# Performance work log

Hardware: AMD Instinct MI355X
Metric: run time of the kernel (lower is better)

Reference implementation:

```python
import math
import jax, jax.numpy as jnp
import numpy as np

B, T, C = 2, 2048, 1024
H = 16
HD = C // H
WIN = 33
HALF = WIN // 2
CAUSAL = True
RADIUS, OMEGA, KSPR, STEP = 6.0, 1.0, 1.0, 0.1
EPS = 1e-8


def _spiral_step(x):
    # x: (..., 3) — the stacked (q, k, v) axis; D=3 -> rotate (x0, x1) pair.
    r = jnp.maximum(jnp.linalg.norm(x, axis=-1, keepdims=True), EPS)
    radial = (RADIUS - r) * (x / r)
    c = jnp.float32(math.cos(OMEGA * STEP))
    s = jnp.float32(math.sin(OMEGA * STEP))
    xi, xj, xl = x[..., 0], x[..., 1], x[..., 2]
    y = jnp.stack([c * xi - s * xj, s * xi + c * xj, xl], axis=-1)
    return x + STEP * (y - x + KSPR * radial)


def setup_inputs() -> dict:
    key = jax.random.key(0)
    ks = jax.random.split(key, 3)
    x = jax.random.normal(ks[0], (B, T, C), dtype=jnp.float32)
    W_attn = jax.random.normal(ks[1], (C, 3 * C), dtype=jnp.float32) * (1.0 / math.sqrt(C))
    W_proj = jax.random.normal(ks[2], (C, C), dtype=jnp.float32) * (1.0 / math.sqrt(C))
    sinks = jnp.zeros((H,), dtype=jnp.float32)
    ln_scale = jnp.ones((1,), dtype=jnp.float32) * 0.9
    ln_delta = jnp.ones((C,), dtype=jnp.float32)
    ln_bias = jnp.zeros((C,), dtype=jnp.float32)
    return {"x": x, "W_attn": W_attn, "W_proj": W_proj, "sinks": sinks,
            "ln_scale": ln_scale, "ln_delta": ln_delta, "ln_bias": ln_bias}


def reference(x, W_attn, W_proj, sinks, ln_scale, ln_delta, ln_bias):
    qkv = x @ W_attn                              # (B,T,3C)
    q, k, v = jnp.split(qkv, 3, axis=-1)          # each (B,T,C)

    # SpiralMix over the stacked (q,k,v) axis, loop_iters=2. Only q,k are
    # taken from the mixed output (v stays the pre-spiral value), matching src.
    s = jnp.stack([q, k, v], axis=-1)             # (B,T,C,3)
    s = _spiral_step(_spiral_step(s))
    q, k = s[..., 0], s[..., 1]

    def to_heads(t):
        return t.reshape(B, T, H, HD).transpose(0, 2, 1, 3)  # (B,H,T,hd)
    q, k, v = to_heads(q), to_heads(k), to_heads(v)

    # local window index
    t_idx = jnp.arange(T)
    offs = jnp.arange(-HALF, HALF + 1)
    neigh = t_idx[:, None] + offs[None, :]                    # (T,W)
    valid = (neigh >= 0) & (neigh < T)
    if CAUSAL:
        valid &= neigh <= t_idx[:, None]
    neigh_c = jnp.clip(neigh, 0, T - 1)

    k_n = k[:, :, neigh_c, :]                                 # (B,H,T,W,hd)
    v_n = v[:, :, neigh_c, :]

    inv_sqrt_d = 1.0 / math.sqrt(HD)
    scores = jnp.einsum('bhtd,bhtwd->bhtw',
                        q.astype(jnp.float32), k_n.astype(jnp.float32)) * inv_sqrt_d
    scores = jnp.where(valid[None, None], scores, -jnp.inf)

    # softmax with learned sink logits per head
    sinks_b = sinks.reshape(1, H, 1, 1).astype(scores.dtype)
    m = jnp.max(scores, axis=-1, keepdims=True)
    mj = jnp.maximum(m, sinks_b)
    exp_s = jnp.exp(scores - mj)
    denom = jnp.sum(exp_s, axis=-1, keepdims=True) + jnp.exp(sinks_b - mj)
    att = exp_s / denom                                       # (B,H,T,W)

    y = jnp.einsum('bhtw,bhtwd->bhtd', att, v_n.astype(att.dtype))
    y = y.transpose(0, 2, 1, 3).reshape(B, T, C).astype(x.dtype)
    y = y @ W_proj
    y = jnp.tanh(ln_scale * y)
    return ln_delta * y + ln_bias
```

## Files before the change

kernel.cpp:

```cpp
#include <hip/hip_runtime.h>
#include <hip/hip_fp16.h>
#include <math.h>

#define T_DIM 2048
#define B_DIM 2
#define C_DIM 1024
#define H_DIM 16
#define M_DIM 4096

typedef _Float16 f16x8 __attribute__((ext_vector_type(8)));
typedef _Float16 f16x4 __attribute__((ext_vector_type(4)));
typedef _Float16 f16x2 __attribute__((ext_vector_type(2)));
typedef float    f32x4 __attribute__((ext_vector_type(4)));

#if defined(__has_builtin)
#  if __has_builtin(__builtin_amdgcn_fdot2)
#    define HAVE_FDOT2 1
#  endif
#endif

static __device__ __forceinline__ float FDOT2(f16x2 a, f16x2 b, float c)
{
#ifdef HAVE_FDOT2
    return __builtin_amdgcn_fdot2(a, b, c, false);
#else
    return c + (float)a[0] * (float)b[0] + (float)a[1] * (float)b[1];
#endif
}

#define ASYNC_COPY16(gsrc, ldst) \
  __builtin_amdgcn_global_load_lds( \
    (__attribute__((address_space(1))) unsigned int*)(gsrc), \
    (__attribute__((address_space(3))) unsigned int*)(ldst), 16, 0, 0)

__global__ __launch_bounds__(256) void conv_x_kernel(const float* __restrict__ x,
                                                     _Float16* __restrict__ xh, int n4)
{
    int i = blockIdx.x * 256 + threadIdx.x;
    if (i >= n4) return;
    float4 v = ((const float4*)x)[i];
    f16x4 o;
    o[0] = (_Float16)v.x; o[1] = (_Float16)v.y;
    o[2] = (_Float16)v.z; o[3] = (_Float16)v.w;
    ((f16x4*)xh)[i] = o;
}

__global__ __launch_bounds__(256) void transpose_f16_kernel(const float* __restrict__ W,
                                                            _Float16* __restrict__ WT,
                                                            int K, int N)
{
    __shared__ float tile[32][33];
    const int nbk = K >> 5;
    const int bk = blockIdx.x % nbk;
    const int bn = blockIdx.x / nbk;
    const int tx = threadIdx.x & 31, ty = threadIdx.x >> 5;
#pragma unroll
    for (int r = ty; r < 32; r += 8)
        tile[r][tx] = W[(long)(bk * 32 + r) * N + bn * 32 + tx];
    __syncthreads();
#pragma unroll
    for (int r = ty; r < 32; r += 8)
        WT[(long)(bn * 32 + r) * K + bk * 32 + tx] = (_Float16)tile[tx][r];
}

template<int EPI>
__global__ __launch_bounds__(256) void gemm_f16_kernel(
    const _Float16* __restrict__ A, const _Float16* __restrict__ Bt,
    float* __restrict__ C, int M, int N, int K,
    const float* __restrict__ ln_scale, const float* __restrict__ ln_delta,
    const float* __restrict__ ln_bias)
{
    __shared__ __attribute__((aligned(16))) _Float16 As[128 * 32];
    __shared__ __attribute__((aligned(16))) _Float16 Bs[128 * 32];

    const int tid  = threadIdx.x;
    const int lane = tid & 63;
    const int wave = tid >> 6;
    const int wr = wave >> 1, wc = wave & 1;
    const int ntn = N >> 7;
    const int m0 = (blockIdx.x / ntn) << 7;
    const int n0 = (blockIdx.x % ntn) << 7;

    f32x4 acc[4][4] = {};

    const int off0 = (wave << 10) + (lane << 4);
    const int e0 = off0 >> 1;
    const int e1 = e0 + 2048;
    const int r0 = e0 >> 5, c0 = e0 & 31;
    const int r1 = r0 + 64, c1 = c0;

    const _Float16* a0 = A  + (long)(m0 + r0) * K + c0;
    const _Float16* a1 = A  + (long)(m0 + r1) * K + c1;
    const _Float16* b0 = Bt + (long)(n0 + r0) * K + c0;
    const _Float16* b1 = Bt + (long)(n0 + r1) * K + c1;

    const int fr = lane & 15;
    const int kb = (lane >> 4) << 3;

    for (int k0 = 0; k0 < K; k0 += 32) {
        __syncthreads();
        ASYNC_COPY16(a0 + k0, As + e0);
        ASYNC_COPY16(a1 + k0, As + e1);
        ASYNC_COPY16(b0 + k0, Bs + e0);
        ASYNC_COPY16(b1 + k0, Bs + e1);
        __syncthreads();

        f16x8 af[4], bf[4];
#pragma unroll
        for (int i = 0; i < 4; i++)
            af[i] = *(const f16x8*)&As[(((wr << 6) + (i << 4) + fr) << 5) + kb];
#pragma unroll
        for (int j = 0; j < 4; j++)
            bf[j] = *(const f16x8*)&Bs[(((wc << 6) + (j << 4) + fr) << 5) + kb];
#pragma unroll
        for (int i = 0; i < 4; i++)
#pragma unroll
            for (int j = 0; j < 4; j++)
                acc[i][j] = __builtin_amdgcn_mfma_f32_16x16x32_f16(af[i], bf[j], acc[i][j], 0, 0, 0);
    }

    const int rsub = (lane >> 4) << 2;
    const float lsc = EPI ? ln_scale[0] : 0.f;
#pragma unroll
    for (int j = 0; j < 4; j++) {
        const int col = n0 + (wc << 6) + (j << 4) + fr;
        float ld = 0.f, lb = 0.f;
        if (EPI) { ld = ln_delta[col]; lb = ln_bias[col]; }
#pragma unroll
        for (int i = 0; i < 4; i++) {
            const int rbase = m0 + (wr << 6) + (i << 4) + rsub;
#pragma unroll
            for (int r = 0; r < 4; r++) {
                float v = acc[i][j][r];
                if (EPI) v = ld * tanhf(lsc * v) + lb;
                C[(long)(rbase + r) * N + col] = v;
            }
        }
    }
}

__device__ __forceinline__ void spiral2(float& xi, float& xj, float xl)
{
    const float CS = 0.9950041652780258f;
    const float SN = 0.09983341664682815f;
#pragma unroll
    for (int s = 0; s < 2; s++) {
        float r = sqrtf(xi * xi + xj * xj + xl * xl);
        r = fmaxf(r, 1e-8f);
        const float coef = (6.0f - r) / r;
        const float yi = CS * xi - SN * xj;
        const float yj = SN * xi + CS * xj;
        const float nxi = xi + 0.1f * (yi - xi + coef * xi);
        const float nxj = xj + 0.1f * (yj - xj + coef * xj);
        const float nxl = xl + 0.1f * (coef * xl);
        xi = nxi; xj = nxj; xl = nxl;
    }
}

#define TB   128
#define ROWS 144
#define LDR  68

__global__ __launch_bounds__(128) void attn_kernel(const float* __restrict__ qkv,
                                                   const float* __restrict__ sinks,
                                                   _Float16* __restrict__ yh)
{
    __shared__ __attribute__((aligned(16))) _Float16 k_lds[ROWS * LDR];
    __shared__ __attribute__((aligned(16))) _Float16 v_lds[ROWS * LDR];
    __shared__ __attribute__((aligned(16))) _Float16 q_lds[TB * LDR];

    const int tid = threadIdx.x;
    const int chunk = blockIdx.x & 15;
    const int h = (blockIdx.x >> 4) & 15;
    const int b = blockIdx.x >> 8;
    const int t0 = chunk * TB;
    const long bT = (long)b * T_DIM;

    for (int s = tid; s < ROWS * 4; s += 128) {
        const int ri = s >> 2, q4 = s & 3;
        const int gr = min(max(t0 - 16 + ri, 0), T_DIM - 1);
        const float* base = qkv + (bT + gr) * 3072 + (h << 6) + (q4 << 4);
        float qq[16], kk[16], vv[16];
#pragma unroll
        for (int u = 0; u < 4; u++) {
            *(float4*)&qq[u * 4] = *(const float4*)(base + u * 4);
            *(float4*)&kk[u * 4] = *(const float4*)(base + 1024 + u * 4);
            *(float4*)&vv[u * 4] = *(const float4*)(base + 2048 + u * 4);
        }
#pragma unroll
        for (int u = 0; u < 16; u++) spiral2(qq[u], kk[u], vv[u]);
        const int lbase = ri * LDR + (q4 << 4);
#pragma unroll
        for (int u = 0; u < 8; u++) {
            f16x2 kp; kp[0] = (_Float16)kk[2 * u]; kp[1] = (_Float16)kk[2 * u + 1];
            *(f16x2*)&k_lds[lbase + 2 * u] = kp;
            f16x2 vp; vp[0] = (_Float16)vv[2 * u]; vp[1] = (_Float16)vv[2 * u + 1];
            *(f16x2*)&v_lds[lbase + 2 * u] = vp;
        }
        if (ri >= 16) {
            const int qbase = (ri - 16) * LDR + (q4 << 4);
#pragma unroll
            for (int u = 0; u < 8; u++) {
                f16x2 qp;
                qp[0] = (_Float16)(qq[2 * u] * 0.125f);
                qp[1] = (_Float16)(qq[2 * u + 1] * 0.125f);
                *(f16x2*)&q_lds[qbase + 2 * u] = qp;
            }
        }
    }
    __syncthreads();

    float sc[17];
#pragma unroll
    for (int j = 0; j < 17; j++) sc[j] = 0.f;
    {
        const _Float16* qrow = &q_lds[tid * LDR];
        const _Float16* krow = &k_lds[tid * LDR];
        for (int dd = 0; dd < 32; ++dd) {
            f16x2 q2 = *(const f16x2*)(qrow + 2 * dd);
#pragma unroll
            for (int j = 0; j < 17; j++) {
                f16x2 k2 = *(const f16x2*)(krow + j * LDR + 2 * dd);
                sc[j] = FDOT2(q2, k2, sc[j]);
            }
        }
    }
    __syncthreads();

    const int t = t0 + tid;
#pragma unroll
    for (int j = 0; j < 17; j++)
        if (j + t < 16) sc[j] = -INFINITY;
    const float sink = sinks[h];
    float m = sink;
#pragma unroll
    for (int j = 0; j < 17; j++) m = fmaxf(m, sc[j]);
    float e[17];
    float denom = expf(sink - m);
#pragma unroll
    for (int j = 0; j < 17; j++) { e[j] = expf(sc[j] - m); denom += e[j]; }
    const float rden = 1.f / denom;
#pragma unroll
    for (int j = 0; j < 17; j++) e[j] *= rden;

    float yacc[64];
#pragma unroll
    for (int d = 0; d < 64; d++) yacc[d] = 0.f;
    {
        const _Float16* vrow = &v_lds[tid * LDR];
        for (int j = 0; j < 17; j++) {
            const float a = e[j];
            const _Float16* vr = vrow + j * LDR;
#pragma unroll
            for (int dd = 0; dd < 32; dd++) {
                f16x2 v2 = *(const f16x2*)(vr + 2 * dd);
                yacc[2 * dd]     += a * (float)v2[0];
                yacc[2 * dd + 1] += a * (float)v2[1];
            }
        }
    }

#pragma unroll
    for (int dd = 0; dd < 32; dd++) {
        f16x2 yp; yp[0] = (_Float16)yacc[2 * dd]; yp[1] = (_Float16)yacc[2 * dd + 1];
        *(f16x2*)&q_lds[tid * LDR + 2 * dd] = yp;
    }
    __syncthreads();
    const int w = tid & 31, rb = tid >> 5;
    _Float16* ybase = yh + (bT + t0) * 1024 + (h << 6);
#pragma unroll
    for (int it = 0; it < 32; it++) {
        const int r = (it << 2) + rb;
        *(unsigned int*)(ybase + (long)r * 1024 + (w << 1)) =
            *(const unsigned int*)&q_lds[r * LDR + (w << 1)];
    }
}

extern "C" void kernel_launch(void* const* d_in, const int* in_sizes, int n_in,
                              void* d_out, int out_size, void* d_ws, size_t ws_size,
                              hipStream_t stream)
{
    const float* x        = (const float*)d_in[0];
    const float* W_attn   = (const float*)d_in[1];
    const float* W_proj   = (const float*)d_in[2];
    const float* sinks    = (const float*)d_in[3];
    const float* ln_scale = (const float*)d_in[4];
    const float* ln_delta = (const float*)d_in[5];
    const float* ln_bias  = (const float*)d_in[6];
    float* out = (float*)d_out;

    char* ws = (char*)d_ws;
    _Float16* xh  = (_Float16*)(ws);
    _Float16* WaT = (_Float16*)(ws + (size_t)( 8u << 20));
    _Float16* WpT = (_Float16*)(ws + (size_t)(14u << 20));
    float*    qkv = (float*)   (ws + (size_t)(16u << 20));
    _Float16* yh  = (_Float16*)(ws + (size_t)(64u << 20));

    conv_x_kernel<<<4096, 256, 0, stream>>>(x, xh, 1048576);
    transpose_f16_kernel<<<(1024 / 32) * (3072 / 32), 256, 0, stream>>>(W_attn, WaT, 1024, 3072);
    transpose_f16_kernel<<<(1024 / 32) * (1024 / 32), 256, 0, stream>>>(W_proj, WpT, 1024, 1024);
    gemm_f16_kernel<0><<<32 * 24, 256, 0, stream>>>(xh, WaT, qkv, 4096, 3072, 1024,
                                                    nullptr, nullptr, nullptr);
    attn_kernel<<<512, 128, 0, stream>>>(qkv, sinks, yh);
    gemm_f16_kernel<1><<<32 * 8, 256, 0, stream>>>(yh, WpT, out, 4096, 1024, 1024,
                                                   ln_scale, ln_delta, ln_bias);
}
```

Before: 198.3 us.

## Double-buffer GEMM, emit fp16 qkv, vectorize attention LDS access, retile projection

The GEMM kernel now double-buffers its A/B tiles in LDS so the next K-slice loads while MFMAs run on the current one, and it raises wave priority around the MFMA block. The QKV GEMM writes fp16 instead of fp32, which halves that intermediate's write and read traffic but rounds q/k/v to fp16 before the spiral step. The attention kernel changes its LDS row padding and reads and writes LDS and global memory with 16-byte vectors. The output projection uses a 64-row tile so it launches twice as many blocks.

```diff
diff --git a/kernel.cpp b/kernel.cpp
--- a/kernel.cpp
+++ b/kernel.cpp
@@ -12,6 +12,8 @@
 typedef _Float16 f16x4 __attribute__((ext_vector_type(4)));
 typedef _Float16 f16x2 __attribute__((ext_vector_type(2)));
 typedef float    f32x4 __attribute__((ext_vector_type(4)));
+
+union f16x8_u { f16x8 v; f16x2 h[4]; _Float16 e[8]; };
 
 #if defined(__has_builtin)
 #  if __has_builtin(__builtin_amdgcn_fdot2)
@@ -63,60 +65,81 @@
         WT[(long)(bn * 32 + r) * K + bk * 32 + tx] = (_Float16)tile[tx][r];
 }
 
-template<int EPI>
+template<int BM, int EPI, int OUTF16>
 __global__ __launch_bounds__(256) void gemm_f16_kernel(
     const _Float16* __restrict__ A, const _Float16* __restrict__ Bt,
-    float* __restrict__ C, int M, int N, int K,
+    void* __restrict__ Cv, int M, int N, int K,
     const float* __restrict__ ln_scale, const float* __restrict__ ln_delta,
     const float* __restrict__ ln_bias)
 {
-    __shared__ __attribute__((aligned(16))) _Float16 As[128 * 32];
-    __shared__ __attribute__((aligned(16))) _Float16 Bs[128 * 32];
+    constexpr int M_REP   = BM / 32;
+    constexpr int A_LOADS = BM / 64;
+    __shared__ __attribute__((aligned(16))) _Float16 As[2][BM * 32];
+    __shared__ __attribute__((aligned(16))) _Float16 Bs[2][128 * 32];
 
     const int tid  = threadIdx.x;
     const int lane = tid & 63;
     const int wave = tid >> 6;
     const int wr = wave >> 1, wc = wave & 1;
     const int ntn = N >> 7;
-    const int m0 = (blockIdx.x / ntn) << 7;
+    const int m0 = (blockIdx.x / ntn) * BM;
     const int n0 = (blockIdx.x % ntn) << 7;
 
-    f32x4 acc[4][4] = {};
-
-    const int off0 = (wave << 10) + (lane << 4);
-    const int e0 = off0 >> 1;
-    const int e1 = e0 + 2048;
-    const int r0 = e0 >> 5, c0 = e0 & 31;
-    const int r1 = r0 + 64, c1 = c0;
-
-    const _Float16* a0 = A  + (long)(m0 + r0) * K + c0;
-    const _Float16* a1 = A  + (long)(m0 + r1) * K + c1;
-    const _Float16* b0 = Bt + (long)(n0 + r0) * K + c0;
-    const _Float16* b1 = Bt + (long)(n0 + r1) * K + c1;
+    f32x4 acc[M_REP][4] = {};
+
+    const int ea = tid * 8;
+    const _Float16* aptr[A_LOADS];
+    const _Float16* bptr[2];
+#pragma unroll
+    for (int l = 0; l < A_LOADS; ++l) {
+        const int e = ea + l * 2048;
+        aptr[l] = A + (long)(m0 + (e >> 5)) * K + (e & 31);
+    }
+#pragma unroll
+    for (int l = 0; l < 2; ++l) {
+        const int e = ea + l * 2048;
+        bptr[l] = Bt + (long)(n0 + (e >> 5)) * K + (e & 31);
+    }
 
     const int fr = lane & 15;
     const int kb = (lane >> 4) << 3;
-
-    for (int k0 = 0; k0 < K; k0 += 32) {
-        __syncthreads();
-        ASYNC_COPY16(a0 + k0, As + e0);
-        ASYNC_COPY16(a1 + k0, As + e1);
-        ASYNC_COPY16(b0 + k0, Bs + e0);
-        ASYNC_COPY16(b1 + k0, Bs + e1);
-        __syncthreads();
-
-        f16x8 af[4], bf[4];
-#pragma unroll
-        for (int i = 0; i < 4; i++)
-            af[i] = *(const f16x8*)&As[(((wr << 6) + (i << 4) + fr) << 5) + kb];
+    const int NT = K >> 5;
+
+#pragma unroll
+    for (int l = 0; l < A_LOADS; ++l) ASYNC_COPY16(aptr[l], &As[0][ea + l * 2048]);
+#pragma unroll
+    for (int l = 0; l < 2; ++l)       ASYNC_COPY16(bptr[l], &Bs[0][ea + l * 2048]);
+    asm volatile("s_waitcnt vmcnt(0)" ::: "memory");
+    __syncthreads();
+
+    int cur = 0;
+    for (int t = 0; t < NT; ++t) {
+        if (t + 1 < NT) {
+            const int k0 = (t + 1) << 5;
+#pragma unroll
+            for (int l = 0; l < A_LOADS; ++l) ASYNC_COPY16(aptr[l] + k0, &As[cur ^ 1][ea + l * 2048]);
+#pragma unroll
+            for (int l = 0; l < 2; ++l)       ASYNC_COPY16(bptr[l] + k0, &Bs[cur ^ 1][ea + l * 2048]);
+        }
+        f16x8 af[M_REP], bf[4];
+#pragma unroll
+        for (int i = 0; i < M_REP; i++)
+            af[i] = *(const f16x8*)&As[cur][((wr * (BM / 2) + (i << 4) + fr) << 5) + kb];
 #pragma unroll
         for (int j = 0; j < 4; j++)
-            bf[j] = *(const f16x8*)&Bs[(((wc << 6) + (j << 4) + fr) << 5) + kb];
-#pragma unroll
-        for (int i = 0; i < 4; i++)
+            bf[j] = *(const f16x8*)&Bs[cur][(((wc << 6) + (j << 4) + fr) << 5) + kb];
+        __builtin_amdgcn_s_setprio(1);
+#pragma unroll
+        for (int i = 0; i < M_REP; i++)
 #pragma unroll
             for (int j = 0; j < 4; j++)
                 acc[i][j] = __builtin_amdgcn_mfma_f32_16x16x32_f16(af[i], bf[j], acc[i][j], 0, 0, 0);
+        __builtin_amdgcn_s_setprio(0);
+        if (t + 1 < NT) {
+            asm volatile("s_waitcnt vmcnt(0)" ::: "memory");
+            __syncthreads();
+            cur ^= 1;
+        }
     }
 
     const int rsub = (lane >> 4) << 2;
@@ -127,13 +150,14 @@
         float ld = 0.f, lb = 0.f;
         if (EPI) { ld = ln_delta[col]; lb = ln_bias[col]; }
 #pragma unroll
-        for (int i = 0; i < 4; i++) {
-            const int rbase = m0 + (wr << 6) + (i << 4) + rsub;
+        for (int i = 0; i < M_REP; i++) {
+            const int rbase = m0 + wr * (BM / 2) + (i << 4) + rsub;
 #pragma unroll
             for (int r = 0; r < 4; r++) {
                 float v = acc[i][j][r];
                 if (EPI) v = ld * tanhf(lsc * v) + lb;
-                C[(long)(rbase + r) * N + col] = v;
+                if (OUTF16) ((_Float16*)Cv)[(long)(rbase + r) * N + col] = (_Float16)v;
+                else        ((float*)Cv)[(long)(rbase + r) * N + col] = v;
             }
         }
     }
@@ -159,9 +183,9 @@
 
 #define TB   128
 #define ROWS 144
-#define LDR  68
-
-__global__ __launch_bounds__(128) void attn_kernel(const float* __restrict__ qkv,
+#define LDR  72
+
+__global__ __launch_bounds__(128) void attn_kernel(const _Float16* __restrict__ qkv,
                                                    const float* __restrict__ sinks,
                                                    _Float16* __restrict__ yh)
 {
@@ -179,53 +203,62 @@
     for (int s = tid; s < ROWS * 4; s += 128) {
         const int ri = s >> 2, q4 = s & 3;
         const int gr = min(max(t0 - 16 + ri, 0), T_DIM - 1);
-        const float* base = qkv + (bT + gr) * 3072 + (h << 6) + (q4 << 4);
+        const _Float16* base = qkv + (bT + gr) * 3072 + (h << 6) + (q4 << 4);
+        f16x8_u qa, qb, ka, kb2, va, vb;
+        qa.v  = *(const f16x8*)(base);        qb.v  = *(const f16x8*)(base + 8);
+        ka.v  = *(const f16x8*)(base + 1024); kb2.v = *(const f16x8*)(base + 1032);
+        va.v  = *(const f16x8*)(base + 2048); vb.v  = *(const f16x8*)(base + 2056);
         float qq[16], kk[16], vv[16];
 #pragma unroll
-        for (int u = 0; u < 4; u++) {
-            *(float4*)&qq[u * 4] = *(const float4*)(base + u * 4);
-            *(float4*)&kk[u * 4] = *(const float4*)(base + 1024 + u * 4);
-            *(float4*)&vv[u * 4] = *(const float4*)(base + 2048 + u * 4);
+        for (int u = 0; u < 8; u++) {
+            qq[u] = (float)qa.e[u]; qq[8 + u] = (float)qb.e[u];
+            kk[u] = (float)ka.e[u]; kk[8 + u] = (float)kb2.e[u];
+            vv[u] = (float)va.e[u]; vv[8 + u] = (float)vb.e[u];
         }
 #pragma unroll
         for (int u = 0; u < 16; u++) spiral2(qq[u], kk[u], vv[u]);
         const int lbase = ri * LDR + (q4 << 4);
+        f16x8_u ko0, ko1, vo0, vo1;
 #pragma unroll
         for (int u = 0; u < 8; u++) {
-            f16x2 kp; kp[0] = (_Float16)kk[2 * u]; kp[1] = (_Float16)kk[2 * u + 1];
-            *(f16x2*)&k_lds[lbase + 2 * u] = kp;
-            f16x2 vp; vp[0] = (_Float16)vv[2 * u]; vp[1] = (_Float16)vv[2 * u + 1];
-            *(f16x2*)&v_lds[lbase + 2 * u] = vp;
-        }
+            ko0.e[u] = (_Float16)kk[u]; ko1.e[u] = (_Float16)kk[8 + u];
+            vo0.e[u] = (_Float16)vv[u]; vo1.e[u] = (_Float16)vv[8 + u];
+        }
+        *(f16x8*)&k_lds[lbase]     = ko0.v;
+        *(f16x8*)&k_lds[lbase + 8] = ko1.v;
+        *(f16x8*)&v_lds[lbase]     = vo0.v;
+        *(f16x8*)&v_lds[lbase + 8] = vo1.v;
         if (ri >= 16) {
             const int qbase = (ri - 16) * LDR + (q4 << 4);
+            f16x8_u qo0, qo1;
 #pragma unroll
             for (int u = 0; u < 8; u++) {
-                f16x2 qp;
-                qp[0] = (_Float16)(qq[2 * u] * 0.125f);
-                qp[1] = (_Float16)(qq[2 * u + 1] * 0.125f);
-                *(f16x2*)&q_lds[qbase + 2 * u] = qp;
+                qo0.e[u] = (_Float16)(qq[u] * 0.125f);
+                qo1.e[u] = (_Float16)(qq[8 + u] * 0.125f);
             }
+            *(f16x8*)&q_lds[qbase]     = qo0.v;
+            *(f16x8*)&q_lds[qbase + 8] = qo1.v;
         }
     }
     __syncthreads();
 
+    f16x8_u qv[8];
+#pragma unroll
+    for (int u = 0; u < 8; u++) qv[u].v = *(const f16x8*)&q_lds[tid * LDR + u * 8];
+
     float sc[17];
 #pragma unroll
-    for (int j = 0; j < 17; j++) sc[j] = 0.f;
-    {
-        const _Float16* qrow = &q_lds[tid * LDR];
-        const _Float16* krow = &k_lds[tid * LDR];
-        for (int dd = 0; dd < 32; ++dd) {
-            f16x2 q2 = *(const f16x2*)(qrow + 2 * dd);
-#pragma unroll
-            for (int j = 0; j < 17; j++) {
-                f16x2 k2 = *(const f16x2*)(krow + j * LDR + 2 * dd);
-                sc[j] = FDOT2(q2, k2, sc[j]);
-            }
-        }
-    }
-    __syncthreads();
+    for (int j = 0; j < 17; j++) {
+        const _Float16* kr = &k_lds[(tid + j) * LDR];
+        float s = 0.f;
+#pragma unroll
+        for (int u = 0; u < 8; u++) {
+            f16x8_u kx; kx.v = *(const f16x8*)&kr[u * 8];
+#pragma unroll
+            for (int p = 0; p < 4; p++) s = FDOT2(qv[u].h[p], kx.h[p], s);
+        }
+        sc[j] = s;
+    }
 
     const int t = t0 + tid;
 #pragma unroll
@@ -246,33 +279,32 @@
     float yacc[64];
 #pragma unroll
     for (int d = 0; d < 64; d++) yacc[d] = 0.f;
-    {
-        const _Float16* vrow = &v_lds[tid * LDR];
-        for (int j = 0; j < 17; j++) {
-            const float a = e[j];
-            const _Float16* vr = vrow + j * LDR;
-#pragma unroll
-            for (int dd = 0; dd < 32; dd++) {
-                f16x2 v2 = *(const f16x2*)(vr + 2 * dd);
-                yacc[2 * dd]     += a * (float)v2[0];
-                yacc[2 * dd + 1] += a * (float)v2[1];
-            }
-        }
-    }
-
-#pragma unroll
-    for (int dd = 0; dd < 32; dd++) {
-        f16x2 yp; yp[0] = (_Float16)yacc[2 * dd]; yp[1] = (_Float16)yacc[2 * dd + 1];
-        *(f16x2*)&q_lds[tid * LDR + 2 * dd] = yp;
+#pragma unroll
+    for (int j = 0; j < 17; j++) {
+        const float a = e[j];
+        const _Float16* vr = &v_lds[(tid + j) * LDR];
+#pragma unroll
+        for (int u = 0; u < 8; u++) {
+            f16x8_u vx; vx.v = *(const f16x8*)&vr[u * 8];
+#pragma unroll
+            for (int z = 0; z < 8; z++) yacc[u * 8 + z] += a * (float)vx.e[z];
+        }
+    }
+
+#pragma unroll
+    for (int u = 0; u < 8; u++) {
+        f16x8_u yo;
+#pragma unroll
+        for (int z = 0; z < 8; z++) yo.e[z] = (_Float16)yacc[u * 8 + z];
+        *(f16x8*)&q_lds[tid * LDR + u * 8] = yo.v;
     }
     __syncthreads();
-    const int w = tid & 31, rb = tid >> 5;
-    _Float16* ybase = yh + (bT + t0) * 1024 + (h << 6);
-#pragma unroll
-    for (int it = 0; it < 32; it++) {
-        const int r = (it << 2) + rb;
-        *(unsigned int*)(ybase + (long)r * 1024 + (w << 1)) =
-            *(const unsigned int*)&q_lds[r * LDR + (w << 1)];
+    const int ch = tid & 7, rb = tid >> 3;
+#pragma unroll
+    for (int pass = 0; pass < 8; ++pass) {
+        const int r = pass * 16 + rb;
+        *(f16x8*)(yh + (bT + t0 + r) * 1024 + (h << 6) + ch * 8) =
+            *(const f16x8*)&q_lds[r * LDR + ch * 8];
     }
 }
 
@@ -290,18 +322,18 @@
     float* out = (float*)d_out;
 
     char* ws = (char*)d_ws;
-    _Float16* xh  = (_Float16*)(ws);
-    _Float16* WaT = (_Float16*)(ws + (size_t)( 8u << 20));
-    _Float16* WpT = (_Float16*)(ws + (size_t)(14u << 20));
-    float*    qkv = (float*)   (ws + (size_t)(16u << 20));
-    _Float16* yh  = (_Float16*)(ws + (size_t)(64u << 20));
+    _Float16* xh    = (_Float16*)(ws);
+    _Float16* WaT   = (_Float16*)(ws + (size_t)( 8u << 20));
+    _Float16* WpT   = (_Float16*)(ws + (size_t)(14u << 20));
+    _Float16* qkv16 = (_Float16*)(ws + (size_t)(16u << 20));
+    _Float16* yh    = (_Float16*)(ws + (size_t)(40u << 20));
 
     conv_x_kernel<<<4096, 256, 0, stream>>>(x, xh, 1048576);
     transpose_f16_kernel<<<(1024 / 32) * (3072 / 32), 256, 0, stream>>>(W_attn, WaT, 1024, 3072);
     transpose_f16_kernel<<<(1024 / 32) * (1024 / 32), 256, 0, stream>>>(W_proj, WpT, 1024, 1024);
-    gemm_f16_kernel<0><<<32 * 24, 256, 0, stream>>>(xh, WaT, qkv, 4096, 3072, 1024,
-                                                    nullptr, nullptr, nullptr);
-    attn_kernel<<<512, 128, 0, stream>>>(qkv, sinks, yh);
-    gemm_f16_kernel<1><<<32 * 8, 256, 0, stream>>>(yh, WpT, out, 4096, 1024, 1024,
-                                                   ln_scale, ln_delta, ln_bias);
-}
+    gemm_f16_kernel<128, 0, 1><<<32 * 24, 256, 0, stream>>>(xh, WaT, qkv16, 4096, 3072, 1024,
+                                                            nullptr, nullptr, nullptr);
+    attn_kernel<<<512, 128, 0, stream>>>(qkv16, sinks, yh);
+    gemm_f16_kernel<64, 1, 0><<<64 * 8, 256, 0, stream>>>(yh, WpT, out, 4096, 1024, 1024,
+                                                          ln_scale, ln_delta, ln_bias);
+}
```

Measured after the change: 182.6 us. -7.9%, faster.
